# Performance work log

Hardware: AMD Instinct MI355X
Metric: run time of the kernel (lower is better)

The kernel has to match this reference:

```python
import jax, jax.numpy as jnp
import numpy as np

B, L, D = 8, 512, 1024
NUM_SPANS = 6144  # L * max_width


def setup_inputs() -> dict:
    key = jax.random.key(0)
    k_h, k_s, k_w, k_b = jax.random.split(key, 4)
    h = jax.random.normal(k_h, (B, L, D), dtype=jnp.float32)
    span_idx = jax.random.randint(k_s, (B, NUM_SPANS, 2), 0, L, dtype=jnp.int64)
    # Linear(hidden, hidden) params (xavier-ish scale)
    lim = float(np.sqrt(6.0 / (D + D)))
    W = jax.random.uniform(k_w, (D, D), dtype=jnp.float32, minval=-lim, maxval=lim)
    b = jnp.zeros((D,), dtype=jnp.float32)
    return {"h": h, "span_idx": span_idx, "W": W, "b": b}


def reference(h, span_idx, W, b):
    # h: [B, L, D]; span_idx: [B, S, 2] with S = L * width
    Bb, Ll, Dd = h.shape
    start = jnp.clip(span_idx[..., 0], 0, Ll - 1)  # [B, S]
    end = jnp.clip(span_idx[..., 1], 0, Ll - 1)    # [B, S]
    valid = start <= end                            # [B, S]
    # prefix sums: cs[i, t] = sum_{u < t} h[i, u]  -> [B, L+1, D]
    cs = jnp.concatenate([jnp.zeros((Bb, 1, Dd), h.dtype), jnp.cumsum(h, axis=1)], axis=1)
    span_sum = (jnp.take_along_axis(cs, (end + 1)[:, :, None], axis=1)
                - jnp.take_along_axis(cs, start[:, :, None], axis=1))  # [B, S, D]
    count = (end - start + 1).astype(h.dtype)[:, :, None]
    span_rep = jnp.where(valid[:, :, None], span_sum / count, 0.0)  # [B, S, D]
    out = jax.nn.relu(jnp.einsum('bsd,ed->bse', span_rep, W) + b)
    return out.reshape(Bb, Ll, -1, Dd)
```

## Files before the change

kernel.cpp:

```cpp
#include <hip/hip_runtime.h>
#include <hip/hip_bf16.h>
#include <stdint.h>

#define B_DIM 8
#define L_DIM 512
#define D_DIM 1024
#define S_DIM 6144
#define NCHUNK 8
#define CHUNK (L_DIM / NCHUNK)
#define CSB (513 * 1024)

typedef __attribute__((ext_vector_type(8))) short short8;
typedef __attribute__((ext_vector_type(4))) float f32x4;
typedef __attribute__((ext_vector_type(8))) unsigned short us8;

__device__ __forceinline__ unsigned short bf16b(float x) {
    __hip_bfloat16 h = __float2bfloat16(x);
    return *reinterpret_cast<unsigned short*>(&h);
}

__device__ __forceinline__ unsigned short f2bf(float f) {
    unsigned int u = __float_as_uint(f);
    u += 0x7FFFu + ((u >> 16) & 1u);
    return (unsigned short)(u >> 16);
}

__global__ __launch_bounds__(256) void chunk_sums(const float* __restrict__ h,
                                                  float* __restrict__ csum) {
    int tid = blockIdx.x * 256 + threadIdx.x;
    int d = tid & 1023;
    int c = (tid >> 10) & 7;
    int b = tid >> 13;
    const float* hp = h + ((size_t)b * L_DIM + c * CHUNK) * D_DIM + d;
    float s = 0.f;
    #pragma unroll 8
    for (int i = 0; i < CHUNK; ++i) s += hp[(size_t)i * D_DIM];
    csum[tid] = s;
}

__global__ __launch_bounds__(256) void build_cs(const float* __restrict__ h,
                                                const float* __restrict__ csum,
                                                float* __restrict__ cs) {
    int tid = blockIdx.x * 256 + threadIdx.x;
    int d = tid & 1023;
    int c = (tid >> 10) & 7;
    int b = tid >> 13;
    float p = 0.f;
    for (int cc = 0; cc < c; ++cc)
        p += csum[(b << 13) + (cc << 10) + d];
    const float* hp = h + ((size_t)b * L_DIM + c * CHUNK) * D_DIM + d;
    float* cp = cs + ((size_t)b * (L_DIM + 1) + c * CHUNK) * D_DIM + d;
    if (c == 0) cp[0] = 0.f;
    #pragma unroll 8
    for (int i = 0; i < CHUNK; ++i) {
        p += hp[(size_t)i * D_DIM];
        cp[(size_t)(i + 1) * D_DIM] = p;
    }
}

__global__ __launch_bounds__(256) void wconv(const float* __restrict__ W,
                                             unsigned short* __restrict__ Wbf) {
    int tid = blockIdx.x * 256 + threadIdx.x;
    const float4* p = (const float4*)(W + (size_t)tid * 8);
    float4 a = p[0], c = p[1];
    us8 o;
    o[0] = f2bf(a.x); o[1] = f2bf(a.y); o[2] = f2bf(a.z); o[3] = f2bf(a.w);
    o[4] = f2bf(c.x); o[5] = f2bf(c.y); o[6] = f2bf(c.z); o[7] = f2bf(c.w);
    *(us8*)&Wbf[(size_t)tid * 8] = o;
}

__global__ __launch_bounds__(512, 2) void fused_gemm(
    const float* __restrict__ cs,
    const int* __restrict__ span_idx,
    const unsigned short* __restrict__ Wbf,
    const float* __restrict__ bias,
    float* __restrict__ out) {
    constexpr int K = D_DIM, N = D_DIM;
    __shared__ __align__(16) unsigned short As[2][128 * 64];
    __shared__ __align__(16) unsigned short Bs[2][256 * 64];
    __shared__ int sOffS[128];
    __shared__ int sOffE[128];
    __shared__ float sInv[128];

    const int tid = threadIdx.x;
    const int wid = tid >> 6, lane = tid & 63;
    const int widbase = wid << 6;

    int blk = blockIdx.x;
    int swz = (blk & 7) * 192 + (blk >> 3);
    const int bm = swz >> 2;
    const int bn = swz & 3;
    const int rowM = bm * 128;
    const int colN = bn * 256;
    const int b = bm / 48;
    const float* csb = cs + (size_t)b * CSB;

    if (tid < 128) {
        int2 se = ((const int2*)span_idx)[rowM + tid];
        int st = min(max(se.x, 0), L_DIM - 1);
        int en = min(max(se.y, 0), L_DIM - 1);
        float inv = (st <= en) ? 1.0f / (float)(en - st + 1) : 0.0f;
        sOffS[tid] = st << 10;
        sOffE[tid] = (en + 1) << 10;
        sInv[tid] = inv;
    }
    __syncthreads();

    const int ar0 = tid >> 3;
    const int ac8 = tid & 7;
    const float* pS0 = csb + sOffS[ar0] + ac8 * 8;
    const float* pE0 = csb + sOffE[ar0] + ac8 * 8;
    const float inv0 = sInv[ar0];
    const float* pS1 = csb + sOffS[ar0 + 64] + ac8 * 8;
    const float* pE1 = csb + sOffE[ar0 + 64] + ac8 * 8;
    const float inv1 = sInv[ar0 + 64];
    const int wa0 = ar0 * 128 + ((ac8 * 16) ^ ((ar0 & 7) << 4));
    const int wa1 = (ar0 + 64) * 128 + ((ac8 * 16) ^ ((ar0 & 7) << 4));

    const int fr = lane & 15;
    const int kq = lane >> 4;
    const int wr = wid >> 2, wc = wid & 3;

    f32x4 acc[4][4];
    #pragma unroll
    for (int i = 0; i < 4; ++i)
        #pragma unroll
        for (int j = 0; j < 4; ++j) acc[i][j] = (f32x4){0.f, 0.f, 0.f, 0.f};

    float4 eA0, eA1, sA0, sA1, eB0, eB1, sB0, sB1;

#define CS_LOAD(k0v) do { \
        eA0 = *(const float4*)(pE0 + (k0v));     eA1 = *(const float4*)(pE0 + (k0v) + 4); \
        sA0 = *(const float4*)(pS0 + (k0v));     sA1 = *(const float4*)(pS0 + (k0v) + 4); \
        eB0 = *(const float4*)(pE1 + (k0v));     eB1 = *(const float4*)(pE1 + (k0v) + 4); \
        sB0 = *(const float4*)(pS1 + (k0v));     sB1 = *(const float4*)(pS1 + (k0v) + 4); \
    } while (0)

#define A_WRITE(bufi) do { \
        us8 o0, o1; \
        o0[0] = bf16b((eA0.x - sA0.x) * inv0); o0[1] = bf16b((eA0.y - sA0.y) * inv0); \
        o0[2] = bf16b((eA0.z - sA0.z) * inv0); o0[3] = bf16b((eA0.w - sA0.w) * inv0); \
        o0[4] = bf16b((eA1.x - sA1.x) * inv0); o0[5] = bf16b((eA1.y - sA1.y) * inv0); \
        o0[6] = bf16b((eA1.z - sA1.z) * inv0); o0[7] = bf16b((eA1.w - sA1.w) * inv0); \
        o1[0] = bf16b((eB0.x - sB0.x) * inv1); o1[1] = bf16b((eB0.y - sB0.y) * inv1); \
        o1[2] = bf16b((eB0.z - sB0.z) * inv1); o1[3] = bf16b((eB0.w - sB0.w) * inv1); \
        o1[4] = bf16b((eB1.x - sB1.x) * inv1); o1[5] = bf16b((eB1.y - sB1.y) * inv1); \
        o1[6] = bf16b((eB1.z - sB1.z) * inv1); o1[7] = bf16b((eB1.w - sB1.w) * inv1); \
        *(us8*)((char*)As[bufi] + wa0) = o0; \
        *(us8*)((char*)As[bufi] + wa1) = o1; \
    } while (0)

#define STAGE_B(k0v, bufi) do { \
        _Pragma("unroll") \
        for (int i = 0; i < 4; ++i) { \
            int ci = i * 512 + tid; \
            int rB = ci >> 3, cB = ci & 7; \
            const unsigned short* srcB = Wbf + (size_t)(colN + rB) * K + (k0v) + ((cB ^ (rB & 7)) * 8); \
            __builtin_amdgcn_global_load_lds( \
                (const __attribute__((address_space(1))) void*)srcB, \
                (__attribute__((address_space(3))) void*)&Bs[bufi][(i * 512 + widbase) * 8], \
                16, 0, 0); \
        } \
    } while (0)

#define COMPUTE(bufi) do { \
        _Pragma("unroll") \
        for (int ks = 0; ks < 2; ++ks) { \
            const int kb = ks * 64 + kq * 16; \
            short8 af[4], bq[4]; \
            _Pragma("unroll") \
            for (int i = 0; i < 4; ++i) { \
                int ra = wr * 64 + i * 16 + fr; \
                af[i] = *(const short8*)((const char*)As[bufi] + ra * 128 + (kb ^ ((ra & 7) << 4))); \
                int rb = wc * 64 + i * 16 + fr; \
                bq[i] = *(const short8*)((const char*)Bs[bufi] + rb * 128 + (kb ^ ((rb & 7) << 4))); \
            } \
            _Pragma("unroll") \
            for (int i = 0; i < 4; ++i) \
                _Pragma("unroll") \
                for (int j = 0; j < 4; ++j) \
                    acc[i][j] = __builtin_amdgcn_mfma_f32_16x16x32_bf16(af[i], bq[j], acc[i][j], 0, 0, 0); \
        } \
    } while (0)

    STAGE_B(0, 0);
    CS_LOAD(0);
    A_WRITE(0);
    __syncthreads();

    int buf = 0;
    for (int t = 0; t < 16; ++t) {
        if (t < 15) {
            STAGE_B((t + 1) * 64, buf ^ 1);
            CS_LOAD((t + 1) * 64);
        }
        COMPUTE(buf);
        if (t < 15) A_WRITE(buf ^ 1);
        __syncthreads();
        buf ^= 1;
    }

    const int m0 = rowM + wr * 64;
    const int n0 = colN + wc * 64;
    float bv[4];
    #pragma unroll
    for (int j = 0; j < 4; ++j) bv[j] = bias[n0 + j * 16 + fr];
    #pragma unroll
    for (int i = 0; i < 4; ++i)
        #pragma unroll
        for (int j = 0; j < 4; ++j)
            #pragma unroll
            for (int r = 0; r < 4; ++r) {
                int m = m0 + i * 16 + kq * 4 + r;
                int n = n0 + j * 16 + fr;
                float v = acc[i][j][r] + bv[j];
                out[(size_t)m * N + n] = v > 0.f ? v : 0.f;
            }
#undef CS_LOAD
#undef A_WRITE
#undef STAGE_B
#undef COMPUTE
}

extern "C" void kernel_launch(void* const* d_in, const int* in_sizes, int n_in,
                              void* d_out, int out_size, void* d_ws, size_t ws_size,
                              hipStream_t stream) {
    const float* h = (const float*)d_in[0];
    const int* span = (const int*)d_in[1];
    const float* W = (const float*)d_in[2];
    const float* bias = (const float*)d_in[3];
    float* out = (float*)d_out;

    char* ws = (char*)d_ws;
    float* cs = (float*)(ws);
    unsigned short* Wbf = (unsigned short*)(ws + 16809984);
    float* csum = (float*)(ws + 18907136);

    chunk_sums<<<256, 256, 0, stream>>>(h, csum);
    build_cs<<<256, 256, 0, stream>>>(h, csum, cs);
    wconv<<<512, 256, 0, stream>>>(W, Wbf);
    fused_gemm<<<1536, 512, 0, stream>>>(cs, span, Wbf, bias, out);
}
```

Baseline: 383.3 us.

## Single-buffer A tile, prefetch B two steps ahead, raise occupancy hint

Cuts LDS use by keeping a single A tile buffer and drops the shared span-offset tables, computing each thread's span bounds directly in registers. The launch bound is raised to request four blocks per CU. The loop now takes two barriers per iteration: A is rewritten only after compute finishes, and B loads are issued two k-steps ahead into the freed buffer. The goal is more resident waves to hide gather latency, at the cost of an extra barrier per iteration, serialized A writes, and tighter register limits that may cause spills.

```diff
diff --git a/kernel.cpp b/kernel.cpp
--- a/kernel.cpp
+++ b/kernel.cpp
@@ -69,18 +69,15 @@
     *(us8*)&Wbf[(size_t)tid * 8] = o;
 }
 
-__global__ __launch_bounds__(512, 2) void fused_gemm(
+__global__ __launch_bounds__(512, 4) void fused_gemm(
     const float* __restrict__ cs,
     const int* __restrict__ span_idx,
     const unsigned short* __restrict__ Wbf,
     const float* __restrict__ bias,
     float* __restrict__ out) {
     constexpr int K = D_DIM, N = D_DIM;
-    __shared__ __align__(16) unsigned short As[2][128 * 64];
+    __shared__ __align__(16) unsigned short As[128 * 64];
     __shared__ __align__(16) unsigned short Bs[2][256 * 64];
-    __shared__ int sOffS[128];
-    __shared__ int sOffE[128];
-    __shared__ float sInv[128];
 
     const int tid = threadIdx.x;
     const int wid = tid >> 6, lane = tid & 63;
@@ -95,25 +92,18 @@
     const int b = bm / 48;
     const float* csb = cs + (size_t)b * CSB;
 
-    if (tid < 128) {
-        int2 se = ((const int2*)span_idx)[rowM + tid];
-        int st = min(max(se.x, 0), L_DIM - 1);
-        int en = min(max(se.y, 0), L_DIM - 1);
-        float inv = (st <= en) ? 1.0f / (float)(en - st + 1) : 0.0f;
-        sOffS[tid] = st << 10;
-        sOffE[tid] = (en + 1) << 10;
-        sInv[tid] = inv;
-    }
-    __syncthreads();
-
     const int ar0 = tid >> 3;
     const int ac8 = tid & 7;
-    const float* pS0 = csb + sOffS[ar0] + ac8 * 8;
-    const float* pE0 = csb + sOffE[ar0] + ac8 * 8;
-    const float inv0 = sInv[ar0];
-    const float* pS1 = csb + sOffS[ar0 + 64] + ac8 * 8;
-    const float* pE1 = csb + sOffE[ar0 + 64] + ac8 * 8;
-    const float inv1 = sInv[ar0 + 64];
+    int2 se0 = ((const int2*)span_idx)[rowM + ar0];
+    int2 se1 = ((const int2*)span_idx)[rowM + ar0 + 64];
+    int st0 = min(max(se0.x, 0), L_DIM - 1), en0 = min(max(se0.y, 0), L_DIM - 1);
+    int st1 = min(max(se1.x, 0), L_DIM - 1), en1 = min(max(se1.y, 0), L_DIM - 1);
+    const float inv0 = (st0 <= en0) ? 1.0f / (float)(en0 - st0 + 1) : 0.0f;
+    const float inv1 = (st1 <= en1) ? 1.0f / (float)(en1 - st1 + 1) : 0.0f;
+    const float* pS0 = csb + (st0 << 10) + ac8 * 8;
+    const float* pE0 = csb + ((en0 + 1) << 10) + ac8 * 8;
+    const float* pS1 = csb + (st1 << 10) + ac8 * 8;
+    const float* pE1 = csb + ((en1 + 1) << 10) + ac8 * 8;
     const int wa0 = ar0 * 128 + ((ac8 * 16) ^ ((ar0 & 7) << 4));
     const int wa1 = (ar0 + 64) * 128 + ((ac8 * 16) ^ ((ar0 & 7) << 4));
 
@@ -136,7 +126,7 @@
         sB0 = *(const float4*)(pS1 + (k0v));     sB1 = *(const float4*)(pS1 + (k0v) + 4); \
     } while (0)
 
-#define A_WRITE(bufi) do { \
+#define A_WRITE() do { \
         us8 o0, o1; \
         o0[0] = bf16b((eA0.x - sA0.x) * inv0); o0[1] = bf16b((eA0.y - sA0.y) * inv0); \
         o0[2] = bf16b((eA0.z - sA0.z) * inv0); o0[3] = bf16b((eA0.w - sA0.w) * inv0); \
@@ -146,8 +136,8 @@
         o1[2] = bf16b((eB0.z - sB0.z) * inv1); o1[3] = bf16b((eB0.w - sB0.w) * inv1); \
         o1[4] = bf16b((eB1.x - sB1.x) * inv1); o1[5] = bf16b((eB1.y - sB1.y) * inv1); \
         o1[6] = bf16b((eB1.z - sB1.z) * inv1); o1[7] = bf16b((eB1.w - sB1.w) * inv1); \
-        *(us8*)((char*)As[bufi] + wa0) = o0; \
-        *(us8*)((char*)As[bufi] + wa1) = o1; \
+        *(us8*)((char*)As + wa0) = o0; \
+        *(us8*)((char*)As + wa1) = o1; \
     } while (0)
 
 #define STAGE_B(k0v, bufi) do { \
@@ -171,7 +161,7 @@
             _Pragma("unroll") \
             for (int i = 0; i < 4; ++i) { \
                 int ra = wr * 64 + i * 16 + fr; \
-                af[i] = *(const short8*)((const char*)As[bufi] + ra * 128 + (kb ^ ((ra & 7) << 4))); \
+                af[i] = *(const short8*)((const char*)As + ra * 128 + (kb ^ ((ra & 7) << 4))); \
                 int rb = wc * 64 + i * 16 + fr; \
                 bq[i] = *(const short8*)((const char*)Bs[bufi] + rb * 128 + (kb ^ ((rb & 7) << 4))); \
             } \
@@ -183,21 +173,19 @@
         } \
     } while (0)
 
+    CS_LOAD(0);
     STAGE_B(0, 0);
-    CS_LOAD(0);
-    A_WRITE(0);
+    A_WRITE();
     __syncthreads();
-
-    int buf = 0;
+    STAGE_B(64, 1);
+
     for (int t = 0; t < 16; ++t) {
-        if (t < 15) {
-            STAGE_B((t + 1) * 64, buf ^ 1);
-            CS_LOAD((t + 1) * 64);
-        }
-        COMPUTE(buf);
-        if (t < 15) A_WRITE(buf ^ 1);
+        if (t < 15) CS_LOAD((t + 1) * 64);
+        COMPUTE(t & 1);
         __syncthreads();
-        buf ^= 1;
+        if (t < 15) A_WRITE();
+        __syncthreads();
+        if (t < 14) STAGE_B((t + 2) * 64, t & 1);
     }
 
     const int m0 = rowM + wr * 64;
```

Result: no change. 381.6 us (-0.4%).
